# Kernel tuning notes

Measured on AMD Instinct MI355X. Metric: run time of the kernel, lower is better.

## Reference

```python
import jax, jax.numpy as jnp
import numpy as np

B, H, L, T, V = 32, 1024, 128, 127, 32000


def setup_inputs() -> dict:
    key = jax.random.key(0)
    ks = jax.random.split(key, 16)
    s = 1.0 / np.sqrt(H)
    return {
        "word_indices": jax.random.randint(ks[0], (B,), 0, V),
        "last_hidden": jax.random.normal(ks[1], (1, B, H), jnp.float32),
        "tanh_hidden": jax.random.normal(ks[2], (B, H), jnp.float32),
        "tree_output": jax.random.normal(ks[3], (T, B, H), jnp.float32),
        "seq_output": jax.random.normal(ks[4], (L, B, H), jnp.float32),
        "numNode": jax.random.randint(ks[5], (B,), 0, T),
        "emb_table": jax.random.normal(ks[6], (V, H), jnp.float32) * 0.02,
        "W_ih": jax.random.uniform(ks[7], (4 * H, H), jnp.float32, -s, s),
        "W_hh": jax.random.uniform(ks[8], (4 * H, H), jnp.float32, -s, s),
        "b_ih": jax.random.uniform(ks[9], (4 * H,), jnp.float32, -s, s),
        "b_hh": jax.random.uniform(ks[10], (4 * H,), jnp.float32, -s, s),
        "W_comb": jax.random.uniform(ks[11], (H, 2 * H), jnp.float32, -s, s),
        "b_comb": jax.random.uniform(ks[12], (H,), jnp.float32, -s, s),
        "W_out": jax.random.uniform(ks[13], (V, H), jnp.float32, -s, s),
        "b_out": jax.random.uniform(ks[14], (V,), jnp.float32, -s, s),
    }


def _lstm_cell(x, h, c, W_ih, W_hh, b_ih, b_hh):
    gates = x @ W_ih.T + b_ih + h @ W_hh.T + b_hh  # (B, 4H)
    i, f, g, o = jnp.split(gates, 4, axis=-1)      # torch gate order i,f,g,o
    i, f, o = jax.nn.sigmoid(i), jax.nn.sigmoid(f), jax.nn.sigmoid(o)
    c1 = f * c + i * jnp.tanh(g)
    return o * jnp.tanh(c1), c1


def reference(word_indices, last_hidden, tanh_hidden, tree_output, seq_output,
              numNode, emb_table, W_ih, W_hh, b_ih, b_hh, W_comb, b_comb,
              W_out, b_out):
    tree = jnp.transpose(tree_output, (1, 0, 2))  # (B,T,H)
    seq = jnp.transpose(seq_output, (1, 0, 2))    # (B,L,H)
    lhidden = last_hidden[0]                       # (B,H)

    # LSTM step (skipped if all word indices are 0 == begin token)
    emb = emb_table[word_indices]                  # (B,H)
    h0 = lhidden + tanh_hidden
    c0 = jnp.zeros_like(h0)
    h1, _ = _lstm_cell(emb, h0, c0, W_ih, W_hh, b_ih, b_hh)
    is_begin = jnp.sum(word_indices) == 0
    cur = jnp.where(is_begin, lhidden, h1)         # (B,H)

    # Ragged attention over concat(seq[:numLeaf], tree[:numNode]) via masking
    enc = jnp.concatenate([seq, tree], axis=1)     # (B, L+T, H)
    pos = jnp.arange(L + T)
    numLeaf = numNode + 1
    mask = jnp.where(pos[None, :] < L,
                     pos[None, :] < numLeaf[:, None],
                     (pos[None, :] - L) < numNode[:, None])  # (B, L+T)
    scores = jnp.einsum('bh,bth->bt', cur, enc)
    scores = jnp.where(mask, scores, -1e30)
    w = jax.nn.softmax(scores, axis=1)
    context = jnp.einsum('bt,bth->bh', w, enc)     # (B,H)

    tanh_h = jnp.tanh(jnp.concatenate([cur, context], axis=1) @ W_comb.T + b_comb)
    out_vec = tanh_h @ W_out.T + b_out             # (B,V)
    prob = jax.nn.softmax(out_vec, axis=0)         # NOTE: dim=0 as in source
    return prob, cur, tanh_h, context
```

## Files before the change

kernel.cpp:

```cpp
#include <hip/hip_runtime.h>

#define BB 32
#define HH 1024
#define LL 128
#define TT 127
#define VV 32000
#define NT 255

typedef __attribute__((ext_vector_type(8))) short bf16x8;
typedef __attribute__((ext_vector_type(4))) float f32x4;

#define MFMA(a, b, c) __builtin_amdgcn_mfma_f32_16x16x32_bf16((a), (b), (c), 0, 0, 0)

static __device__ __forceinline__ short f2bf(float f) {
  unsigned u = __builtin_bit_cast(unsigned, f);
  u += 0x7fffu + ((u >> 16) & 1u);
  return (short)(u >> 16);
}

static __device__ __forceinline__ bf16x8 load_cvt8(const float* __restrict__ p) {
  f32x4 a = *(const f32x4*)p;
  f32x4 b = *(const f32x4*)(p + 4);
  bf16x8 r;
  r[0]=f2bf(a[0]); r[1]=f2bf(a[1]); r[2]=f2bf(a[2]); r[3]=f2bf(a[3]);
  r[4]=f2bf(b[0]); r[5]=f2bf(b[1]); r[6]=f2bf(b[2]); r[7]=f2bf(b[3]);
  return r;
}

static __device__ __forceinline__ bf16x8 load_add_cvt8(const float* __restrict__ p,
                                                       const float* __restrict__ q) {
  f32x4 a = *(const f32x4*)p, a2 = *(const f32x4*)(p + 4);
  f32x4 b = *(const f32x4*)q, b2 = *(const f32x4*)(q + 4);
  bf16x8 r;
  r[0]=f2bf(a[0]+b[0]); r[1]=f2bf(a[1]+b[1]); r[2]=f2bf(a[2]+b[2]); r[3]=f2bf(a[3]+b[3]);
  r[4]=f2bf(a2[0]+b2[0]); r[5]=f2bf(a2[1]+b2[1]); r[6]=f2bf(a2[2]+b2[2]); r[7]=f2bf(a2[3]+b2[3]);
  return r;
}

__global__ __launch_bounds__(64) void k_gates(
    const int* __restrict__ wi, const float* __restrict__ lh,
    const float* __restrict__ th, const float* __restrict__ emb,
    const float* __restrict__ W_ih, const float* __restrict__ W_hh,
    float* __restrict__ pgates)
{
  int lane = threadIdx.x;
  int tile = blockIdx.x >> 2;
  int ks   = blockIdx.x & 3;
  int al = lane & 15, ah = lane >> 4;
  int cg = tile * 16 + al;
  int g  = (cg < 1024) ? cg : cg + 1024;
  const float* W = (ks < 2) ? W_ih : W_hh;
  int kbase = (ks & 1) * 512;
  const float* Arow = W + (size_t)g * HH + kbase + ah * 8;
  f32x4 acc_lo = {0.f,0.f,0.f,0.f}, acc_hi = {0.f,0.f,0.f,0.f};

  if (ks < 2) {
    const float* e_lo = emb + (size_t)wi[al] * HH + kbase + ah * 8;
    const float* e_hi = emb + (size_t)wi[al + 16] * HH + kbase + ah * 8;
    #pragma unroll 4
    for (int kk = 0; kk < 16; ++kk) {
      bf16x8 a = load_cvt8(Arow + kk * 32);
      acc_lo = MFMA(a, load_cvt8(e_lo + kk * 32), acc_lo);
      acc_hi = MFMA(a, load_cvt8(e_hi + kk * 32), acc_hi);
    }
  } else {
    const float* p_lo = lh + al * HH + kbase + ah * 8;
    const float* q_lo = th + al * HH + kbase + ah * 8;
    const float* p_hi = lh + (al + 16) * HH + kbase + ah * 8;
    const float* q_hi = th + (al + 16) * HH + kbase + ah * 8;
    #pragma unroll 4
    for (int kk = 0; kk < 16; ++kk) {
      bf16x8 a = load_cvt8(Arow + kk * 32);
      acc_lo = MFMA(a, load_add_cvt8(p_lo + kk * 32, q_lo + kk * 32), acc_lo);
      acc_hi = MFMA(a, load_add_cvt8(p_hi + kk * 32, q_hi + kk * 32), acc_hi);
    }
  }
  float* outp = pgates + ((size_t)ks * 3072 + tile * 16) * 32;
  #pragma unroll
  for (int j = 0; j < 4; ++j) {
    int row = ah * 4 + j;
    outp[row * 32 + al]      = acc_lo[j];
    outp[row * 32 + al + 16] = acc_hi[j];
  }
}

__global__ __launch_bounds__(256) void k_cell(
    const float* __restrict__ pgates, const float* __restrict__ b_ih,
    const float* __restrict__ b_hh, const int* __restrict__ wi,
    const float* __restrict__ lh, float* __restrict__ cur_ws,
    float* __restrict__ out_cur)
{
  __shared__ int s_begin;
  if (threadIdx.x == 0) {
    int s = 0;
    #pragma unroll
    for (int i = 0; i < BB; ++i) s += wi[i];
    s_begin = (s == 0);
  }
  __syncthreads();
  int b = threadIdx.x & 31;
  int h = blockIdx.x * 8 + (threadIdx.x >> 5);
  float iv = 0.f, gv = 0.f, ov = 0.f;
  #pragma unroll
  for (int ks = 0; ks < 4; ++ks) {
    const float* p = pgates + (size_t)ks * 3072 * 32;
    iv += p[(size_t)h * 32 + b];
    gv += p[(size_t)(1024 + h) * 32 + b];
    ov += p[(size_t)(2048 + h) * 32 + b];
  }
  iv += b_ih[h] + b_hh[h];
  gv += b_ih[2048 + h] + b_hh[2048 + h];
  ov += b_ih[3072 + h] + b_hh[3072 + h];
  float ig = 1.f / (1.f + __expf(-iv));
  float og = 1.f / (1.f + __expf(-ov));
  float c1 = ig * tanhf(gv);
  float h1 = og * tanhf(c1);
  float c  = s_begin ? lh[b * HH + h] : h1;
  cur_ws[b * HH + h] = c;
  out_cur[b * HH + h] = c;
}

__global__ __launch_bounds__(256) void k_scores(
    const float* __restrict__ cur, const float* __restrict__ seq,
    const float* __restrict__ tree, const int* __restrict__ numNode,
    float* __restrict__ scores)
{
  int lane = threadIdx.x & 63;
  int gw = blockIdx.x * 4 + (threadIdx.x >> 6);
  if (gw >= BB * NT) return;
  int b = gw & 31, t = gw >> 5;
  int nn = numNode[b];
  int tl    = (t < LL) ? t : (t - LL);
  int limit = (t < LL) ? (nn + 1) : nn;
  if (tl >= limit) { if (lane == 0) scores[b * NT + t] = -1e30f; return; }
  const float* row = (t < LL) ? (seq + ((size_t)t * BB + b) * HH)
                              : (tree + ((size_t)(t - LL) * BB + b) * HH);
  const float* c = cur + b * HH;
  float acc = 0.f;
  #pragma unroll
  for (int ch = 0; ch < 4; ++ch) {
    int k = ch * 256 + lane * 4;
    f32x4 e = *(const f32x4*)(row + k);
    f32x4 q = *(const f32x4*)(c + k);
    acc += e[0]*q[0] + e[1]*q[1] + e[2]*q[2] + e[3]*q[3];
  }
  #pragma unroll
  for (int off = 32; off; off >>= 1) acc += __shfl_xor(acc, off);
  if (lane == 0) scores[b * NT + t] = acc;
}

__global__ __launch_bounds__(256) void k_context(
    const float* __restrict__ scores, const float* __restrict__ seq,
    const float* __restrict__ tree, float* __restrict__ ctx_ws,
    float* __restrict__ out_ctx)
{
  int b  = blockIdx.x >> 4;
  int hc = blockIdx.x & 15;
  int tid = threadIdx.x;
  int lane = tid & 63, wv = tid >> 6;
  __shared__ float w[256];
  __shared__ float red[8];
  __shared__ float part[4][64];

  float s = (tid < NT) ? scores[b * NT + tid] : -1e30f;
  float m = s;
  #pragma unroll
  for (int off = 32; off; off >>= 1) m = fmaxf(m, __shfl_xor(m, off));
  if (lane == 0) red[wv] = m;
  __syncthreads();
  m = fmaxf(fmaxf(red[0], red[1]), fmaxf(red[2], red[3]));
  float e = (tid < NT) ? __expf(s - m) : 0.f;
  float z = e;
  #pragma unroll
  for (int off = 32; off; off >>= 1) z += __shfl_xor(z, off);
  if (lane == 0) red[4 + wv] = z;
  __syncthreads();
  z = red[4] + red[5] + red[6] + red[7];
  w[tid] = e / z;
  __syncthreads();

  int h  = hc * 64 + lane;
  int tc = wv;
  int ntt = (tc == 3) ? 63 : 64;
  const float* base = (tc < 2)
      ? seq + ((size_t)(tc * 64) * BB + b) * HH + h
      : tree + ((size_t)(tc * 64 - LL) * BB + b) * HH + h;
  const float* wp = &w[tc * 64];
  float acc = 0.f;
  #pragma unroll 8
  for (int tt = 0; tt < ntt; ++tt)
    acc += wp[tt] * base[(size_t)tt * (BB * HH)];
  part[tc][lane] = acc;
  __syncthreads();
  if (tc == 0) {
    float v = part[0][lane] + part[1][lane] + part[2][lane] + part[3][lane];
    ctx_ws[b * HH + h] = v;
    out_ctx[b * HH + h] = v;
  }
}

__global__ __launch_bounds__(64) void k_comb(
    const float* __restrict__ W_comb, const float* __restrict__ cur,
    const float* __restrict__ ctx, float* __restrict__ pcomb)
{
  int lane = threadIdx.x;
  int tile = blockIdx.x >> 2;
  int ks   = blockIdx.x & 3;
  int al = lane & 15, ah = lane >> 4;
  int m = tile * 16 + al;
  int kbase = ks * 512;
  const float* Arow = W_comb + (size_t)m * 2048 + kbase + ah * 8;
  const float* X = (ks < 2) ? cur : ctx;
  int xkb = kbase & 1023;
  const float* xlo = X + al * HH + xkb + ah * 8;
  const float* xhi = X + (al + 16) * HH + xkb + ah * 8;
  f32x4 acc_lo = {0.f,0.f,0.f,0.f}, acc_hi = {0.f,0.f,0.f,0.f};
  #pragma unroll 4
  for (int kk = 0; kk < 16; ++kk) {
    bf16x8 a = load_cvt8(Arow + kk * 32);
    acc_lo = MFMA(a, load_cvt8(xlo + kk * 32), acc_lo);
    acc_hi = MFMA(a, load_cvt8(xhi + kk * 32), acc_hi);
  }
  float* outp = pcomb + ((size_t)ks * 1024 + tile * 16) * 32;
  #pragma unroll
  for (int j = 0; j < 4; ++j) {
    int row = ah * 4 + j;
    outp[row * 32 + al]      = acc_lo[j];
    outp[row * 32 + al + 16] = acc_hi[j];
  }
}

__global__ __launch_bounds__(256) void k_combred(
    const float* __restrict__ pcomb, const float* __restrict__ b_comb,
    float* __restrict__ out_th, unsigned short* __restrict__ thb)
{
  int b = threadIdx.x & 31;
  int m = blockIdx.x * 8 + (threadIdx.x >> 5);
  float v = 0.f;
  #pragma unroll
  for (int ks = 0; ks < 4; ++ks) v += pcomb[((size_t)ks * 1024 + m) * 32 + b];
  v = tanhf(v + b_comb[m]);
  out_th[b * HH + m] = v;
  thb[b * HH + m] = (unsigned short)f2bf(v);
}

__global__ __launch_bounds__(256) void k_wout(
    const float* __restrict__ W_out, const unsigned short* __restrict__ thb,
    float* __restrict__ vt)
{
  int lane = threadIdx.x & 63;
  int tile = blockIdx.x * 4 + (threadIdx.x >> 6);
  int al = lane & 15, ah = lane >> 4;
  size_t row = (size_t)tile * 16 + al;
  const float* Arow = W_out + row * HH + ah * 8;
  const unsigned short* blo = thb + al * HH + ah * 8;
  const unsigned short* bhi = thb + (al + 16) * HH + ah * 8;
  f32x4 acc_lo = {0.f,0.f,0.f,0.f}, acc_hi = {0.f,0.f,0.f,0.f};
  #pragma unroll 4
  for (int kk = 0; kk < 32; ++kk) {
    bf16x8 a  = load_cvt8(Arow + kk * 32);
    bf16x8 bl = *(const bf16x8*)(blo + kk * 32);
    bf16x8 bh = *(const bf16x8*)(bhi + kk * 32);
    acc_lo = MFMA(a, bl, acc_lo);
    acc_hi = MFMA(a, bh, acc_hi);
  }
  float* outp = vt + (size_t)tile * 16 * 32;
  #pragma unroll
  for (int j = 0; j < 4; ++j) {
    int r = ah * 4 + j;
    outp[r * 32 + al]      = acc_lo[j];
    outp[r * 32 + al + 16] = acc_hi[j];
  }
}

__global__ __launch_bounds__(256) void k_psoftmax(
    const float* __restrict__ vt, float* __restrict__ prob)
{
  int v = blockIdx.x * 256 + threadIdx.x;
  const float* r = vt + (size_t)v * 32;
  float x[32];
  #pragma unroll
  for (int i = 0; i < 8; ++i) {
    f32x4 t = *(const f32x4*)(r + i * 4);
    x[i*4+0] = t[0]; x[i*4+1] = t[1]; x[i*4+2] = t[2]; x[i*4+3] = t[3];
  }
  float m = x[0];
  #pragma unroll
  for (int i = 1; i < 32; ++i) m = fmaxf(m, x[i]);
  float z = 0.f;
  #pragma unroll
  for (int i = 0; i < 32; ++i) { x[i] = __expf(x[i] - m); z += x[i]; }
  float inv = 1.f / z;
  #pragma unroll
  for (int i = 0; i < 32; ++i) prob[(size_t)i * VV + v] = x[i] * inv;
}

extern "C" void kernel_launch(void* const* d_in, const int* in_sizes, int n_in,
                              void* d_out, int out_size, void* d_ws, size_t ws_size,
                              hipStream_t stream) {
  const int*   wi    = (const int*)d_in[0];
  const float* lh    = (const float*)d_in[1];
  const float* thid  = (const float*)d_in[2];
  const float* tree  = (const float*)d_in[3];
  const float* seq   = (const float*)d_in[4];
  const int*   nn    = (const int*)d_in[5];
  const float* emb   = (const float*)d_in[6];
  const float* Wih   = (const float*)d_in[7];
  const float* Whh   = (const float*)d_in[8];
  const float* bih   = (const float*)d_in[9];
  const float* bhh   = (const float*)d_in[10];
  const float* Wcomb = (const float*)d_in[11];
  const float* bcomb = (const float*)d_in[12];
  const float* Wout  = (const float*)d_in[13];

  float* out = (float*)d_out;
  float* ws  = (float*)d_ws;
  float* pgates = ws;
  float* pcomb  = ws + 393216;
  float* cur    = ws + 524288;
  float* ctx    = ws + 557056;
  float* scores = ws + 589824;
  unsigned short* thb = (unsigned short*)(ws + 598016);
  float* vt     = ws + 614400;

  float* o_prob = out;
  float* o_cur  = out + 1024000;
  float* o_th   = out + 1056768;
  float* o_ctx  = out + 1089536;

  k_gates   <<<dim3(768),  dim3(64),  0, stream>>>(wi, lh, thid, emb, Wih, Whh, pgates);
  k_cell    <<<dim3(128),  dim3(256), 0, stream>>>(pgates, bih, bhh, wi, lh, cur, o_cur);
  k_scores  <<<dim3(2040), dim3(256), 0, stream>>>(cur, seq, tree, nn, scores);
  k_context <<<dim3(512),  dim3(256), 0, stream>>>(scores, seq, tree, ctx, o_ctx);
  k_comb    <<<dim3(256),  dim3(64),  0, stream>>>(Wcomb, cur, ctx, pcomb);
  k_combred <<<dim3(128),  dim3(256), 0, stream>>>(pcomb, bcomb, o_th, thb);
  k_wout    <<<dim3(500),  dim3(256), 0, stream>>>(Wout, thb, vt);
  k_psoftmax<<<dim3(125),  dim3(256), 0, stream>>>(vt, o_prob);
}
```

Measured before the change: 360.4 us.

## Fuse comb reduction and vocab softmax into GEMM kernels, skip masked context rows

The context kernel now bounds each wave's time loop by numNode/numLeaf, so it no longer reads encoder rows whose softmax weight is zero. The combine GEMM does its four K-split partials in one 256-thread block and reduces them through shared memory before applying tanh, which removes the separate reduction kernel. The W_out GEMM computes the column softmax over the batch directly from its MFMA accumulators using lane shuffles. It then writes prob through a shared-memory transpose, which drops the vt round trip and the extra softmax launch. In exchange, k_comb launches only 64 blocks, which lowers parallelism for that GEMM.

```diff
diff --git a/kernel.cpp b/kernel.cpp
--- a/kernel.cpp
+++ b/kernel.cpp
@@ -151,8 +151,8 @@
 
 __global__ __launch_bounds__(256) void k_context(
     const float* __restrict__ scores, const float* __restrict__ seq,
-    const float* __restrict__ tree, float* __restrict__ ctx_ws,
-    float* __restrict__ out_ctx)
+    const float* __restrict__ tree, const int* __restrict__ numNode,
+    float* __restrict__ ctx_ws, float* __restrict__ out_ctx)
 {
   int b  = blockIdx.x >> 4;
   int hc = blockIdx.x & 15;
@@ -181,14 +181,20 @@
 
   int h  = hc * 64 + lane;
   int tc = wv;
-  int ntt = (tc == 3) ? 63 : 64;
+  int nn = numNode[b];
+  int nl = nn + 1;
+  int lim;
+  if      (tc == 0) lim = (nl < 64) ? nl : 64;
+  else if (tc == 1) { lim = nl - 64; lim = (lim < 0) ? 0 : ((lim > 64) ? 64 : lim); }
+  else if (tc == 2) lim = (nn < 64) ? nn : 64;
+  else              { lim = nn - 64; lim = (lim < 0) ? 0 : ((lim > 63) ? 63 : lim); }
   const float* base = (tc < 2)
       ? seq + ((size_t)(tc * 64) * BB + b) * HH + h
       : tree + ((size_t)(tc * 64 - LL) * BB + b) * HH + h;
   const float* wp = &w[tc * 64];
   float acc = 0.f;
-  #pragma unroll 8
-  for (int tt = 0; tt < ntt; ++tt)
+  #pragma unroll 4
+  for (int tt = 0; tt < lim; ++tt)
     acc += wp[tt] * base[(size_t)tt * (BB * HH)];
   part[tc][lane] = acc;
   __syncthreads();
@@ -199,18 +205,19 @@
   }
 }
 
-__global__ __launch_bounds__(64) void k_comb(
+__global__ __launch_bounds__(256) void k_comb(
     const float* __restrict__ W_comb, const float* __restrict__ cur,
-    const float* __restrict__ ctx, float* __restrict__ pcomb)
-{
-  int lane = threadIdx.x;
-  int tile = blockIdx.x >> 2;
-  int ks   = blockIdx.x & 3;
+    const float* __restrict__ ctx, const float* __restrict__ b_comb,
+    float* __restrict__ out_th, unsigned short* __restrict__ thb)
+{
+  int lane = threadIdx.x & 63;
+  int wv   = threadIdx.x >> 6;
+  int tile = blockIdx.x;
   int al = lane & 15, ah = lane >> 4;
   int m = tile * 16 + al;
-  int kbase = ks * 512;
+  int kbase = wv * 512;
   const float* Arow = W_comb + (size_t)m * 2048 + kbase + ah * 8;
-  const float* X = (ks < 2) ? cur : ctx;
+  const float* X = (wv < 2) ? cur : ctx;
   int xkb = kbase & 1023;
   const float* xlo = X + al * HH + xkb + ah * 8;
   const float* xhi = X + (al + 16) * HH + xkb + ah * 8;
@@ -221,35 +228,34 @@
     acc_lo = MFMA(a, load_cvt8(xlo + kk * 32), acc_lo);
     acc_hi = MFMA(a, load_cvt8(xhi + kk * 32), acc_hi);
   }
-  float* outp = pcomb + ((size_t)ks * 1024 + tile * 16) * 32;
+  __shared__ float red[4][16][32];
   #pragma unroll
   for (int j = 0; j < 4; ++j) {
-    int row = ah * 4 + j;
-    outp[row * 32 + al]      = acc_lo[j];
-    outp[row * 32 + al + 16] = acc_hi[j];
-  }
-}
-
-__global__ __launch_bounds__(256) void k_combred(
-    const float* __restrict__ pcomb, const float* __restrict__ b_comb,
-    float* __restrict__ out_th, unsigned short* __restrict__ thb)
-{
-  int b = threadIdx.x & 31;
-  int m = blockIdx.x * 8 + (threadIdx.x >> 5);
-  float v = 0.f;
-  #pragma unroll
-  for (int ks = 0; ks < 4; ++ks) v += pcomb[((size_t)ks * 1024 + m) * 32 + b];
-  v = tanhf(v + b_comb[m]);
-  out_th[b * HH + m] = v;
-  thb[b * HH + m] = (unsigned short)f2bf(v);
+    int r = ah * 4 + j;
+    red[wv][r][al]      = acc_lo[j];
+    red[wv][r][al + 16] = acc_hi[j];
+  }
+  __syncthreads();
+  int tid = threadIdx.x;
+  int ml = tid >> 4, b0 = (tid & 15) * 2;
+  float v0 = red[0][ml][b0]   + red[1][ml][b0]   + red[2][ml][b0]   + red[3][ml][b0];
+  float v1 = red[0][ml][b0+1] + red[1][ml][b0+1] + red[2][ml][b0+1] + red[3][ml][b0+1];
+  int mg = tile * 16 + ml;
+  float bc = b_comb[mg];
+  float t0 = tanhf(v0 + bc), t1 = tanhf(v1 + bc);
+  out_th[b0 * HH + mg]       = t0;
+  out_th[(b0 + 1) * HH + mg] = t1;
+  thb[b0 * HH + mg]       = (unsigned short)f2bf(t0);
+  thb[(b0 + 1) * HH + mg] = (unsigned short)f2bf(t1);
 }
 
 __global__ __launch_bounds__(256) void k_wout(
     const float* __restrict__ W_out, const unsigned short* __restrict__ thb,
-    float* __restrict__ vt)
+    float* __restrict__ prob)
 {
   int lane = threadIdx.x & 63;
-  int tile = blockIdx.x * 4 + (threadIdx.x >> 6);
+  int wv   = threadIdx.x >> 6;
+  int tile = blockIdx.x * 4 + wv;
   int al = lane & 15, ah = lane >> 4;
   size_t row = (size_t)tile * 16 + al;
   const float* Arow = W_out + row * HH + ah * 8;
@@ -264,35 +270,31 @@
     acc_lo = MFMA(a, bl, acc_lo);
     acc_hi = MFMA(a, bh, acc_hi);
   }
-  float* outp = vt + (size_t)tile * 16 * 32;
+  __shared__ float sprob[32][65];
   #pragma unroll
   for (int j = 0; j < 4; ++j) {
-    int r = ah * 4 + j;
-    outp[r * 32 + al]      = acc_lo[j];
-    outp[r * 32 + al + 16] = acc_hi[j];
-  }
-}
-
-__global__ __launch_bounds__(256) void k_psoftmax(
-    const float* __restrict__ vt, float* __restrict__ prob)
-{
-  int v = blockIdx.x * 256 + threadIdx.x;
-  const float* r = vt + (size_t)v * 32;
-  float x[32];
-  #pragma unroll
-  for (int i = 0; i < 8; ++i) {
-    f32x4 t = *(const f32x4*)(r + i * 4);
-    x[i*4+0] = t[0]; x[i*4+1] = t[1]; x[i*4+2] = t[2]; x[i*4+3] = t[3];
-  }
-  float m = x[0];
-  #pragma unroll
-  for (int i = 1; i < 32; ++i) m = fmaxf(m, x[i]);
-  float z = 0.f;
-  #pragma unroll
-  for (int i = 0; i < 32; ++i) { x[i] = __expf(x[i] - m); z += x[i]; }
-  float inv = 1.f / z;
-  #pragma unroll
-  for (int i = 0; i < 32; ++i) prob[(size_t)i * VV + v] = x[i] * inv;
+    float m = fmaxf(acc_lo[j], acc_hi[j]);
+    #pragma unroll
+    for (int mk = 1; mk < 16; mk <<= 1) m = fmaxf(m, __shfl_xor(m, mk));
+    float e0 = __expf(acc_lo[j] - m);
+    float e1 = __expf(acc_hi[j] - m);
+    float z = e0 + e1;
+    #pragma unroll
+    for (int mk = 1; mk < 16; mk <<= 1) z += __shfl_xor(z, mk);
+    float inv = 1.f / z;
+    int vl = wv * 16 + ah * 4 + j;
+    sprob[al][vl]      = e0 * inv;
+    sprob[al + 16][vl] = e1 * inv;
+  }
+  __syncthreads();
+  int tid = threadIdx.x;
+  int b = tid >> 3, vc = (tid & 7) * 8;
+  size_t v0 = (size_t)blockIdx.x * 64 + vc;
+  float* op = prob + (size_t)b * VV + v0;
+  f32x4 w0 = { sprob[b][vc],   sprob[b][vc+1], sprob[b][vc+2], sprob[b][vc+3] };
+  f32x4 w1 = { sprob[b][vc+4], sprob[b][vc+5], sprob[b][vc+6], sprob[b][vc+7] };
+  *(f32x4*)op       = w0;
+  *(f32x4*)(op + 4) = w1;
 }
 
 extern "C" void kernel_launch(void* const* d_in, const int* in_sizes, int n_in,
@@ -316,12 +318,10 @@
   float* out = (float*)d_out;
   float* ws  = (float*)d_ws;
   float* pgates = ws;
-  float* pcomb  = ws + 393216;
-  float* cur    = ws + 524288;
-  float* ctx    = ws + 557056;
-  float* scores = ws + 589824;
-  unsigned short* thb = (unsigned short*)(ws + 598016);
-  float* vt     = ws + 614400;
+  float* cur    = ws + 393216;
+  float* ctx    = ws + 425984;
+  float* scores = ws + 458752;
+  unsigned short* thb = (unsigned short*)(ws + 466944);
 
   float* o_prob = out;
   float* o_cur  = out + 1024000;
@@ -331,9 +331,7 @@
   k_gates   <<<dim3(768),  dim3(64),  0, stream>>>(wi, lh, thid, emb, Wih, Whh, pgates);
   k_cell    <<<dim3(128),  dim3(256), 0, stream>>>(pgates, bih, bhh, wi, lh, cur, o_cur);
   k_scores  <<<dim3(2040), dim3(256), 0, stream>>>(cur, seq, tree, nn, scores);
-  k_context <<<dim3(512),  dim3(256), 0, stream>>>(scores, seq, tree, ctx, o_ctx);
-  k_comb    <<<dim3(256),  dim3(64),  0, stream>>>(Wcomb, cur, ctx, pcomb);
-  k_combred <<<dim3(128),  dim3(256), 0, stream>>>(pcomb, bcomb, o_th, thb);
-  k_wout    <<<dim3(500),  dim3(256), 0, stream>>>(Wout, thb, vt);
-  k_psoftmax<<<dim3(125),  dim3(256), 0, stream>>>(vt, o_prob);
-}
+  k_context <<<dim3(512),  dim3(256), 0, stream>>>(scores, seq, tree, nn, ctx, o_ctx);
+  k_comb    <<<dim3(64),   dim3(256), 0, stream>>>(Wcomb, cur, ctx, bcomb, o_th, thb);
+  k_wout    <<<dim3(500),  dim3(256), 0, stream>>>(Wout, thb, o_prob);
+}
```

After: 355.8 us. No clear change (-1.3%).
